# Kernel tuning notes

Measured on AMD Instinct MI355X. Metric: run time of the kernel, lower is better.

## Reference

```python
import jax, jax.numpy as jnp
import numpy as np

BLOCK_K = 128  # per_1x128 block quantization: block_n=1 (per row), block_k=128


def _dequant(wq, scale):
    # wq: [E, N, K] quantized codes; scale: [E, N, ceil(K/BLOCK_K)]
    K = wq.shape[-1]
    s_full = jnp.repeat(scale, BLOCK_K, axis=-1)[..., :K]
    return wq * s_full


def setup_inputs() -> dict:
    key = jax.random.key(0)
    ks = jax.random.split(key, 6)
    T, E, H, I = 1024, 8, 1024, 768
    x = jax.random.normal(ks[0], (T, H), dtype=jnp.float32)
    router_logits = jax.random.normal(ks[1], (T, E), dtype=jnp.float32)
    # fp8 codes simulated as float values; block scales positive (scale_inv)
    w13_weight = jax.random.normal(ks[2], (E, 2 * I, H), dtype=jnp.float32) * 0.05
    w13_weight_scale_inv = jax.random.uniform(ks[3], (E, 2 * I, H // BLOCK_K), dtype=jnp.float32, minval=0.5, maxval=1.5)
    w2_weight = jax.random.normal(ks[4], (E, H, I), dtype=jnp.float32) * 0.05
    w2_weight_scale_inv = jax.random.uniform(ks[5], (E, H, I // BLOCK_K), dtype=jnp.float32, minval=0.5, maxval=1.5)
    return {
        "x": x,
        "router_logits": router_logits,
        "w13_weight": w13_weight,
        "w13_weight_scale_inv": w13_weight_scale_inv,
        "w2_weight": w2_weight,
        "w2_weight_scale_inv": w2_weight_scale_inv,
        "top_k": 2,
    }


def reference(x, router_logits, w13_weight, w13_weight_scale_inv, w2_weight, w2_weight_scale_inv, top_k):
    T, H = x.shape
    E = router_logits.shape[-1]
    I = w2_weight.shape[-1]

    # ---- dequantize block-scaled weights (inline dequant of fp8 grouped GEMM) ----
    w13 = _dequant(w13_weight, w13_weight_scale_inv)   # [E, 2I, H]
    w2 = _dequant(w2_weight, w2_weight_scale_inv)      # [E, H, I]

    # ---- routing: softmax scoring, top_k, renormalize ----
    probs = jax.nn.softmax(router_logits, axis=-1)     # [T, E]
    topk_w, topk_idx = jax.lax.top_k(probs, top_k)     # [T, K]
    topk_w = topk_w / jnp.sum(topk_w, axis=-1, keepdims=True)  # renormalize=True
    # dense combine weights [T, E] (scatter of top_k routing weights)
    combine = jnp.zeros((T, E), x.dtype).at[jnp.arange(T)[:, None], topk_idx].add(topk_w)

    # ---- grouped expert FFN (dense-over-experts reference) ----
    gate_up = jnp.einsum('th,enh->ten', x, w13)        # [T, E, 2I]
    gate, up = gate_up[..., :I], gate_up[..., I:]
    act = jax.nn.silu(gate) * up                       # silu activation ('silu')
    out_e = jnp.einsum('tei,ehi->teh', act, w2)        # [T, E, H]

    # ---- combine ----
    return jnp.einsum('teh,te->th', out_e, combine)    # [T, H]
```

## Files before the change

### kernel.cpp

```cpp
#include <hip/hip_runtime.h>

#define T_TOK 1024
#define H_DIM 1024
#define I_DIM 768
#define E_NUM 8

#define G13 1572864
#define G2   786432
#define GX   131072
#define GO   131072

typedef __bf16 bf16x8 __attribute__((ext_vector_type(8)));
typedef float  f32x4  __attribute__((ext_vector_type(4)));

__device__ inline void gl2lds16(const void* g, void* l) {
    __builtin_amdgcn_global_load_lds(
        (const __attribute__((address_space(1))) unsigned int*)g,
        (__attribute__((address_space(3))) unsigned int*)l, 16, 0, 0);
}

__device__ inline bf16x8 cvt8(float4 a, float4 b, float s) {
    bf16x8 o;
    o[0] = (__bf16)(a.x * s); o[1] = (__bf16)(a.y * s);
    o[2] = (__bf16)(a.z * s); o[3] = (__bf16)(a.w * s);
    o[4] = (__bf16)(b.x * s); o[5] = (__bf16)(b.y * s);
    o[6] = (__bf16)(b.z * s); o[7] = (__bf16)(b.w * s);
    return o;
}

__global__ __launch_bounds__(256) void prep_kernel(
    const float* __restrict__ w13, const float* __restrict__ w13s,
    const float* __restrict__ w2,  const float* __restrict__ w2s,
    const float* __restrict__ x,   float4* __restrict__ out4,
    __bf16* __restrict__ w13d, __bf16* __restrict__ w2d, __bf16* __restrict__ xbf)
{
    int g = blockIdx.x * 256 + threadIdx.x;
    if (g < G13) {
        int k8 = g & 127;
        int row = g >> 7;
        float s = w13s[(row << 3) | (k8 >> 4)];
        const float4* src = (const float4*)w13 + (size_t)g * 2;
        *(bf16x8*)(w13d + (size_t)g * 8) = cvt8(src[0], src[1], s);
    } else if (g < G13 + G2) {
        int g2 = g - G13;
        unsigned row = (unsigned)g2 / 96u;
        int k8 = g2 - row * 96;
        float s = w2s[row * 6 + (k8 >> 4)];
        const float4* src = (const float4*)w2 + (size_t)g2 * 2;
        *(bf16x8*)(w2d + (size_t)g2 * 8) = cvt8(src[0], src[1], s);
    } else if (g < G13 + G2 + GX) {
        int gx = g - (G13 + G2);
        const float4* src = (const float4*)x + (size_t)gx * 2;
        *(bf16x8*)(xbf + (size_t)gx * 8) = cvt8(src[0], src[1], 1.0f);
    } else {
        int go = g - (G13 + G2 + GX);
        float4 z = make_float4(0.f, 0.f, 0.f, 0.f);
        out4[2 * go] = z; out4[2 * go + 1] = z;
    }
}

__global__ __launch_bounds__(1024) void router_kernel(
    const float* __restrict__ logits,
    int* __restrict__ counts, int* __restrict__ base,
    int* __restrict__ tok_list, float* __restrict__ wt_list)
{
    __shared__ int cnt[E_NUM];
    const int t = threadIdx.x;
    if (t < E_NUM) cnt[t] = 0;
    __syncthreads();
    float l[E_NUM];
#pragma unroll
    for (int e = 0; e < E_NUM; e++) l[e] = logits[t * E_NUM + e];
    int e0 = 0; float m0 = l[0];
#pragma unroll
    for (int e = 1; e < E_NUM; e++) if (l[e] > m0) { m0 = l[e]; e0 = e; }
    int e1 = -1; float m1 = -3e38f;
#pragma unroll
    for (int e = 0; e < E_NUM; e++) if (e != e0 && l[e] > m1) { m1 = l[e]; e1 = e; }
    float w0 = 1.0f / (1.0f + expf(m1 - m0));
    float w1 = 1.0f - w0;
    int p0 = atomicAdd(&cnt[e0], 1);
    tok_list[e0 * T_TOK + p0] = t;
    wt_list[e0 * T_TOK + p0] = w0;
    int p1 = atomicAdd(&cnt[e1], 1);
    tok_list[e1 * T_TOK + p1] = t;
    wt_list[e1 * T_TOK + p1] = w1;
    __syncthreads();
    if (t == 0) {
        int s = 0;
        for (int e = 0; e < E_NUM; e++) { base[e] = s; counts[e] = cnt[e]; s += cnt[e]; }
    }
}

__global__ __launch_bounds__(256, 3) void gemm1_kernel(
    const __bf16* __restrict__ xbf,
    const __bf16* __restrict__ w13d,
    const int* __restrict__ counts,
    const int* __restrict__ base,
    const int* __restrict__ tok_list,
    __bf16* __restrict__ act)
{
    const int e = blockIdx.z;
    const int count = counts[e];
    const int m0 = blockIdx.y * 32;
    if (m0 >= count) return;
    const int n0 = blockIdx.x * 64;
    const int abase = base[e];

    __shared__ union {
        struct {
            __bf16 Bs[2][128 * 64];
            __bf16 Ab[2][32 * 64];
        } s;
        float gu[32 * 132];
    } u;
    __shared__ int tokS[32];

    const int tid = threadIdx.x;
    if (tid < 32) {
        int r = m0 + tid;
        tokS[tid] = (r < count) ? tok_list[e * T_TOK + r] : tok_list[e * T_TOK];
    }
    __syncthreads();

    const int wid = tid >> 6, lane = tid & 63, lrow = lane & 15, quad = lane >> 4;

    const int rA = wid * 8 + (lane >> 3);
    const __bf16* pAst = xbf + (size_t)tokS[rA] * H_DIM + (((lane & 7) ^ (rA & 7)) << 3);
    const __bf16* pBst[4];
#pragma unroll
    for (int i8 = 0; i8 < 4; i8++) {
        int r = wid * 32 + i8 * 8 + (lane >> 3);
        int n = (r < 64) ? (n0 + r) : (I_DIM + n0 + r - 64);
        pBst[i8] = w13d + ((size_t)e * 2 * I_DIM + n) * H_DIM + (((lane & 7) ^ (r & 7)) << 3);
    }

    int aoff[2][2], boff[2][2];
#pragma unroll
    for (int kk = 0; kk < 2; kk++) {
        int gph = ((kk * 4 + quad) ^ (lrow & 7)) << 4;
#pragma unroll
        for (int i = 0; i < 2; i++) {
            aoff[kk][i] = (i * 16 + lrow) * 128 + gph;
            boff[kk][i] = (wid * 32 + i * 16 + lrow) * 128 + gph;
        }
    }

    f32x4 acc[2][2];
#pragma unroll
    for (int i = 0; i < 2; i++)
#pragma unroll
        for (int j = 0; j < 2; j++) { f32x4 z = {0.f, 0.f, 0.f, 0.f}; acc[i][j] = z; }

    auto issue = [&](int b, int k0) {
        gl2lds16(pAst + k0, &u.s.Ab[b][(wid * 8) * 64]);
#pragma unroll
        for (int i8 = 0; i8 < 4; i8++)
            gl2lds16(pBst[i8] + k0, &u.s.Bs[b][(wid * 32 + i8 * 8) * 64]);
    };
    issue(0, 0);

#pragma unroll
    for (int it = 0; it < 16; ++it) {
        const int b = it & 1;
        __syncthreads();
        if (it < 15) issue(b ^ 1, (it + 1) * 64);
        const char* Ab = (const char*)u.s.Ab[b];
        const char* Bb = (const char*)u.s.Bs[b];
#pragma unroll
        for (int kk = 0; kk < 2; kk++) {
            bf16x8 a0 = *(const bf16x8*)(Ab + aoff[kk][0]);
            bf16x8 a1 = *(const bf16x8*)(Ab + aoff[kk][1]);
            bf16x8 b0 = *(const bf16x8*)(Bb + boff[kk][0]);
            bf16x8 b1 = *(const bf16x8*)(Bb + boff[kk][1]);
            acc[0][0] = __builtin_amdgcn_mfma_f32_16x16x32_bf16(a0, b0, acc[0][0], 0, 0, 0);
            acc[1][0] = __builtin_amdgcn_mfma_f32_16x16x32_bf16(a1, b0, acc[1][0], 0, 0, 0);
            acc[0][1] = __builtin_amdgcn_mfma_f32_16x16x32_bf16(a0, b1, acc[0][1], 0, 0, 0);
            acc[1][1] = __builtin_amdgcn_mfma_f32_16x16x32_bf16(a1, b1, acc[1][1], 0, 0, 0);
        }
    }

    __syncthreads();
#pragma unroll
    for (int i = 0; i < 2; i++)
#pragma unroll
        for (int j = 0; j < 2; j++)
#pragma unroll
            for (int r = 0; r < 4; r++) {
                int m = i * 16 + quad * 4 + r;
                int c = wid * 32 + j * 16 + lrow;
                u.gu[m * 132 + c] = acc[i][j][r];
            }
    __syncthreads();

#pragma unroll
    for (int ii = 0; ii < 8; ii++) {
        int o = ii * 256 + tid;
        int m = o >> 6, c = o & 63;
        if (m0 + m < count) {
            float g  = u.gu[m * 132 + c];
            float up = u.gu[m * 132 + 64 + c];
            float a  = g / (1.0f + expf(-g)) * up;
            act[(size_t)(abase + m0 + m) * I_DIM + n0 + c] = (__bf16)a;
        }
    }
}

__global__ __launch_bounds__(256, 3) void gemm2_kernel(
    const __bf16* __restrict__ act,
    const __bf16* __restrict__ w2d,
    const int* __restrict__ counts,
    const int* __restrict__ base,
    const int* __restrict__ tok_list,
    const float* __restrict__ wt_list,
    float* __restrict__ out)
{
    const int e = blockIdx.z;
    const int count = counts[e];
    const int m0 = blockIdx.y * 32;
    if (m0 >= count) return;
    const int n0 = blockIdx.x * 128;
    const int abase = base[e];

    __shared__ struct {
        __bf16 Bs[2][128 * 64];
        __bf16 Ab[2][32 * 64];
    } s;
    __shared__ int   tokS[32];
    __shared__ float wtS[32];

    const int tid = threadIdx.x;
    if (tid < 32) {
        int r = m0 + tid;
        tokS[tid] = (r < count) ? tok_list[e * T_TOK + r] : tok_list[e * T_TOK];
        wtS[tid]  = (r < count) ? wt_list[e * T_TOK + r] : 0.f;
    }
    __syncthreads();

    const int wid = tid >> 6, lane = tid & 63, lrow = lane & 15, quad = lane >> 4;

    const int rA = wid * 8 + (lane >> 3);
    int gr = abase + m0 + rA;
    if (gr > 2 * T_TOK - 1) gr = 2 * T_TOK - 1;
    const __bf16* pAst = act + (size_t)gr * I_DIM + (((lane & 7) ^ (rA & 7)) << 3);
    const __bf16* pBst[4];
#pragma unroll
    for (int i8 = 0; i8 < 4; i8++) {
        int r = wid * 32 + i8 * 8 + (lane >> 3);
        pBst[i8] = w2d + ((size_t)e * H_DIM + n0 + r) * I_DIM + (((lane & 7) ^ (r & 7)) << 3);
    }

    int aoff[2][2], boff[2][2];
#pragma unroll
    for (int kk = 0; kk < 2; kk++) {
        int gph = ((kk * 4 + quad) ^ (lrow & 7)) << 4;
#pragma unroll
        for (int i = 0; i < 2; i++) {
            aoff[kk][i] = (i * 16 + lrow) * 128 + gph;
            boff[kk][i] = (wid * 32 + i * 16 + lrow) * 128 + gph;
        }
    }

    f32x4 acc[2][2];
#pragma unroll
    for (int i = 0; i < 2; i++)
#pragma unroll
        for (int j = 0; j < 2; j++) { f32x4 z = {0.f, 0.f, 0.f, 0.f}; acc[i][j] = z; }

    auto issue = [&](int b, int k0) {
        gl2lds16(pAst + k0, &s.Ab[b][(wid * 8) * 64]);
#pragma unroll
        for (int i8 = 0; i8 < 4; i8++)
            gl2lds16(pBst[i8] + k0, &s.Bs[b][(wid * 32 + i8 * 8) * 64]);
    };
    issue(0, 0);

#pragma unroll
    for (int it = 0; it < 12; ++it) {
        const int b = it & 1;
        __syncthreads();
        if (it < 11) issue(b ^ 1, (it + 1) * 64);
        const char* Ab = (const char*)s.Ab[b];
        const char* Bb = (const char*)s.Bs[b];
#pragma unroll
        for (int kk = 0; kk < 2; kk++) {
            bf16x8 a0 = *(const bf16x8*)(Ab + aoff[kk][0]);
            bf16x8 a1 = *(const bf16x8*)(Ab + aoff[kk][1]);
            bf16x8 b0 = *(const bf16x8*)(Bb + boff[kk][0]);
            bf16x8 b1 = *(const bf16x8*)(Bb + boff[kk][1]);
            acc[0][0] = __builtin_amdgcn_mfma_f32_16x16x32_bf16(a0, b0, acc[0][0], 0, 0, 0);
            acc[1][0] = __builtin_amdgcn_mfma_f32_16x16x32_bf16(a1, b0, acc[1][0], 0, 0, 0);
            acc[0][1] = __builtin_amdgcn_mfma_f32_16x16x32_bf16(a0, b1, acc[0][1], 0, 0, 0);
            acc[1][1] = __builtin_amdgcn_mfma_f32_16x16x32_bf16(a1, b1, acc[1][1], 0, 0, 0);
        }
    }

#pragma unroll
    for (int i = 0; i < 2; i++)
#pragma unroll
        for (int j = 0; j < 2; j++)
#pragma unroll
            for (int r = 0; r < 4; r++) {
                int m = i * 16 + quad * 4 + r;
                if (m0 + m < count) {
                    int h = n0 + wid * 32 + j * 16 + lrow;
                    atomicAdd(&out[(size_t)tokS[m] * H_DIM + h], wtS[m] * acc[i][j][r]);
                }
            }
}

extern "C" void kernel_launch(void* const* d_in, const int* in_sizes, int n_in,
                              void* d_out, int out_size, void* d_ws, size_t ws_size,
                              hipStream_t stream) {
    (void)in_sizes; (void)n_in; (void)out_size; (void)ws_size;
    const float* x      = (const float*)d_in[0];
    const float* logits = (const float*)d_in[1];
    const float* w13    = (const float*)d_in[2];
    const float* w13s   = (const float*)d_in[3];
    const float* w2     = (const float*)d_in[4];
    const float* w2s    = (const float*)d_in[5];
    float* out = (float*)d_out;

    char* ws = (char*)d_ws;
    int*    counts   = (int*)ws;
    int*    base     = (int*)(ws + 128);
    int*    tok_list = (int*)(ws + 256);
    float*  wt_list  = (float*)(ws + 256 + 32768);
    __bf16* act      = (__bf16*)(ws + 65792);
    __bf16* xbf      = (__bf16*)(ws + 65792 + 3145728);
    __bf16* w13d     = (__bf16*)(ws + 65792 + 3145728 + 2097152);
    __bf16* w2d      = (__bf16*)(ws + 65792 + 3145728 + 2097152 + 25165824);

    prep_kernel<<<dim3(10240), 256, 0, stream>>>(w13, w13s, w2, w2s, x,
                                                 (float4*)out, w13d, w2d, xbf);
    router_kernel<<<dim3(1), 1024, 0, stream>>>(logits, counts, base, tok_list, wt_list);
    gemm1_kernel<<<dim3(I_DIM / 64, T_TOK / 32, E_NUM), 256, 0, stream>>>(
        xbf, w13d, counts, base, tok_list, act);
    gemm2_kernel<<<dim3(H_DIM / 128, T_TOK / 32, E_NUM), 256, 0, stream>>>(
        act, w2d, counts, base, tok_list, wt_list, out);
}
```

Before: 162.6 us.

## Replace direct global-to-LDS loads with register-staged double-buffered prefetch in GEMMs

Both grouped GEMM kernels stop using the direct global-to-LDS load builtin. They now prefetch tiles two stages ahead into registers and write them to swizzled LDS with an extra barrier per iteration. Occupancy hints rise from 3 to 4 blocks per CU. In gemm2, token IDs and weights are read straight from global memory in the epilogue instead of staged in shared memory. The intent is deeper latency hiding and higher occupancy, at the cost of more registers, an additional sync per k-step and VGPR-to-LDS store traffic.

```diff
diff --git a/kernel.cpp b/kernel.cpp
--- a/kernel.cpp
+++ b/kernel.cpp
@@ -8,16 +8,9 @@
 #define G13 1572864
 #define G2   786432
 #define GX   131072
-#define GO   131072
 
 typedef __bf16 bf16x8 __attribute__((ext_vector_type(8)));
 typedef float  f32x4  __attribute__((ext_vector_type(4)));
-
-__device__ inline void gl2lds16(const void* g, void* l) {
-    __builtin_amdgcn_global_load_lds(
-        (const __attribute__((address_space(1))) unsigned int*)g,
-        (__attribute__((address_space(3))) unsigned int*)l, 16, 0, 0);
-}
 
 __device__ inline bf16x8 cvt8(float4 a, float4 b, float s) {
     bf16x8 o;
@@ -92,7 +85,9 @@
     }
 }
 
-__global__ __launch_bounds__(256, 3) void gemm1_kernel(
+#define MFMA(A, B, C) __builtin_amdgcn_mfma_f32_16x16x32_bf16(A, B, C, 0, 0, 0)
+
+__global__ __launch_bounds__(256, 4) void gemm1_kernel(
     const __bf16* __restrict__ xbf,
     const __bf16* __restrict__ w13d,
     const int* __restrict__ counts,
@@ -108,33 +103,30 @@
     const int abase = base[e];
 
     __shared__ union {
-        struct {
-            __bf16 Bs[2][128 * 64];
-            __bf16 Ab[2][32 * 64];
-        } s;
+        struct { __bf16 Bs[2][128 * 64]; __bf16 As[2][32 * 64]; } s;
         float gu[32 * 132];
+        int tok[32];
     } u;
-    __shared__ int tokS[32];
 
     const int tid = threadIdx.x;
     if (tid < 32) {
         int r = m0 + tid;
-        tokS[tid] = (r < count) ? tok_list[e * T_TOK + r] : tok_list[e * T_TOK];
-    }
-    __syncthreads();
+        u.tok[tid] = (r < count) ? tok_list[e * T_TOK + r] : tok_list[e * T_TOK];
+    }
+    __syncthreads();
+
+    const int arow = tid >> 3, ag = tid & 7;
+    const __bf16* pA = xbf + (size_t)u.tok[arow] * H_DIM + ag * 8;
+    const int awo = arow * 128 + ((ag ^ (arow & 7)) << 4);
+    const int brow = tid >> 1, bg0 = (tid & 1) * 4;
+    const int nB = (brow < 64) ? (n0 + brow) : (I_DIM + n0 + brow - 64);
+    const __bf16* pB = w13d + ((size_t)e * 2 * I_DIM + nB) * H_DIM + bg0 * 8;
+    int bwo[4];
+#pragma unroll
+    for (int i = 0; i < 4; i++)
+        bwo[i] = brow * 128 + (((bg0 + i) ^ (brow & 7)) << 4);
 
     const int wid = tid >> 6, lane = tid & 63, lrow = lane & 15, quad = lane >> 4;
-
-    const int rA = wid * 8 + (lane >> 3);
-    const __bf16* pAst = xbf + (size_t)tokS[rA] * H_DIM + (((lane & 7) ^ (rA & 7)) << 3);
-    const __bf16* pBst[4];
-#pragma unroll
-    for (int i8 = 0; i8 < 4; i8++) {
-        int r = wid * 32 + i8 * 8 + (lane >> 3);
-        int n = (r < 64) ? (n0 + r) : (I_DIM + n0 + r - 64);
-        pBst[i8] = w13d + ((size_t)e * 2 * I_DIM + n) * H_DIM + (((lane & 7) ^ (r & 7)) << 3);
-    }
-
     int aoff[2][2], boff[2][2];
 #pragma unroll
     for (int kk = 0; kk < 2; kk++) {
@@ -152,20 +144,32 @@
 #pragma unroll
         for (int j = 0; j < 2; j++) { f32x4 z = {0.f, 0.f, 0.f, 0.f}; acc[i][j] = z; }
 
-    auto issue = [&](int b, int k0) {
-        gl2lds16(pAst + k0, &u.s.Ab[b][(wid * 8) * 64]);
-#pragma unroll
-        for (int i8 = 0; i8 < 4; i8++)
-            gl2lds16(pBst[i8] + k0, &u.s.Bs[b][(wid * 32 + i8 * 8) * 64]);
-    };
-    issue(0, 0);
-
-#pragma unroll
+    uint4 rA[2], rB[2][4];
+#pragma unroll
+    for (int s = 0; s < 2; s++) {
+        rA[s] = *(const uint4*)(pA + s * 64);
+#pragma unroll
+        for (int i = 0; i < 4; i++)
+            rB[s][i] = *(const uint4*)(pB + s * 64 + i * 8);
+    }
+
+#pragma unroll 2
     for (int it = 0; it < 16; ++it) {
         const int b = it & 1;
         __syncthreads();
-        if (it < 15) issue(b ^ 1, (it + 1) * 64);
-        const char* Ab = (const char*)u.s.Ab[b];
+        *(uint4*)((char*)u.s.As[b] + awo) = rA[b];
+#pragma unroll
+        for (int i = 0; i < 4; i++)
+            *(uint4*)((char*)u.s.Bs[b] + bwo[i]) = rB[b][i];
+        if (it + 2 < 16) {
+            const int k = (it + 2) * 64;
+            rA[b] = *(const uint4*)(pA + k);
+#pragma unroll
+            for (int i = 0; i < 4; i++)
+                rB[b][i] = *(const uint4*)(pB + k + i * 8);
+        }
+        __syncthreads();
+        const char* Ab = (const char*)u.s.As[b];
         const char* Bb = (const char*)u.s.Bs[b];
 #pragma unroll
         for (int kk = 0; kk < 2; kk++) {
@@ -173,10 +177,10 @@
             bf16x8 a1 = *(const bf16x8*)(Ab + aoff[kk][1]);
             bf16x8 b0 = *(const bf16x8*)(Bb + boff[kk][0]);
             bf16x8 b1 = *(const bf16x8*)(Bb + boff[kk][1]);
-            acc[0][0] = __builtin_amdgcn_mfma_f32_16x16x32_bf16(a0, b0, acc[0][0], 0, 0, 0);
-            acc[1][0] = __builtin_amdgcn_mfma_f32_16x16x32_bf16(a1, b0, acc[1][0], 0, 0, 0);
-            acc[0][1] = __builtin_amdgcn_mfma_f32_16x16x32_bf16(a0, b1, acc[0][1], 0, 0, 0);
-            acc[1][1] = __builtin_amdgcn_mfma_f32_16x16x32_bf16(a1, b1, acc[1][1], 0, 0, 0);
+            acc[0][0] = MFMA(a0, b0, acc[0][0]);
+            acc[1][0] = MFMA(a1, b0, acc[1][0]);
+            acc[0][1] = MFMA(a0, b1, acc[0][1]);
+            acc[1][1] = MFMA(a1, b1, acc[1][1]);
         }
     }
 
@@ -206,7 +210,7 @@
     }
 }
 
-__global__ __launch_bounds__(256, 3) void gemm2_kernel(
+__global__ __launch_bounds__(256, 4) void gemm2_kernel(
     const __bf16* __restrict__ act,
     const __bf16* __restrict__ w2d,
     const int* __restrict__ counts,
@@ -222,34 +226,24 @@
     const int n0 = blockIdx.x * 128;
     const int abase = base[e];
 
-    __shared__ struct {
-        __bf16 Bs[2][128 * 64];
-        __bf16 Ab[2][32 * 64];
-    } s;
-    __shared__ int   tokS[32];
-    __shared__ float wtS[32];
+    __shared__ struct { __bf16 Bs[2][128 * 64]; __bf16 As[2][32 * 64]; } s;
 
     const int tid = threadIdx.x;
-    if (tid < 32) {
-        int r = m0 + tid;
-        tokS[tid] = (r < count) ? tok_list[e * T_TOK + r] : tok_list[e * T_TOK];
-        wtS[tid]  = (r < count) ? wt_list[e * T_TOK + r] : 0.f;
-    }
-    __syncthreads();
+
+    const int arow = tid >> 3, ag = tid & 7;
+    int gr = abase + m0 + arow;
+    if (gr > 2 * T_TOK - 1) gr = 2 * T_TOK - 1;
+    const __bf16* pA = act + (size_t)gr * I_DIM + ag * 8;
+    const int awo = arow * 128 + ((ag ^ (arow & 7)) << 4);
+
+    const int brow = tid >> 1, bg0 = (tid & 1) * 4;
+    const __bf16* pB = w2d + ((size_t)e * H_DIM + n0 + brow) * I_DIM + bg0 * 8;
+    int bwo[4];
+#pragma unroll
+    for (int i = 0; i < 4; i++)
+        bwo[i] = brow * 128 + (((bg0 + i) ^ (brow & 7)) << 4);
 
     const int wid = tid >> 6, lane = tid & 63, lrow = lane & 15, quad = lane >> 4;
-
-    const int rA = wid * 8 + (lane >> 3);
-    int gr = abase + m0 + rA;
-    if (gr > 2 * T_TOK - 1) gr = 2 * T_TOK - 1;
-    const __bf16* pAst = act + (size_t)gr * I_DIM + (((lane & 7) ^ (rA & 7)) << 3);
-    const __bf16* pBst[4];
-#pragma unroll
-    for (int i8 = 0; i8 < 4; i8++) {
-        int r = wid * 32 + i8 * 8 + (lane >> 3);
-        pBst[i8] = w2d + ((size_t)e * H_DIM + n0 + r) * I_DIM + (((lane & 7) ^ (r & 7)) << 3);
-    }
-
     int aoff[2][2], boff[2][2];
 #pragma unroll
     for (int kk = 0; kk < 2; kk++) {
@@ -267,20 +261,32 @@
 #pragma unroll
         for (int j = 0; j < 2; j++) { f32x4 z = {0.f, 0.f, 0.f, 0.f}; acc[i][j] = z; }
 
-    auto issue = [&](int b, int k0) {
-        gl2lds16(pAst + k0, &s.Ab[b][(wid * 8) * 64]);
-#pragma unroll
-        for (int i8 = 0; i8 < 4; i8++)
-            gl2lds16(pBst[i8] + k0, &s.Bs[b][(wid * 32 + i8 * 8) * 64]);
-    };
-    issue(0, 0);
-
-#pragma unroll
+    uint4 rA[2], rB[2][4];
+#pragma unroll
+    for (int sdeep = 0; sdeep < 2; sdeep++) {
+        rA[sdeep] = *(const uint4*)(pA + sdeep * 64);
+#pragma unroll
+        for (int i = 0; i < 4; i++)
+            rB[sdeep][i] = *(const uint4*)(pB + sdeep * 64 + i * 8);
+    }
+
+#pragma unroll 2
     for (int it = 0; it < 12; ++it) {
         const int b = it & 1;
         __syncthreads();
-        if (it < 11) issue(b ^ 1, (it + 1) * 64);
-        const char* Ab = (const char*)s.Ab[b];
+        *(uint4*)((char*)s.As[b] + awo) = rA[b];
+#pragma unroll
+        for (int i = 0; i < 4; i++)
+            *(uint4*)((char*)s.Bs[b] + bwo[i]) = rB[b][i];
+        if (it + 2 < 12) {
+            const int k = (it + 2) * 64;
+            rA[b] = *(const uint4*)(pA + k);
+#pragma unroll
+            for (int i = 0; i < 4; i++)
+                rB[b][i] = *(const uint4*)(pB + k + i * 8);
+        }
+        __syncthreads();
+        const char* Ab = (const char*)s.As[b];
         const char* Bb = (const char*)s.Bs[b];
 #pragma unroll
         for (int kk = 0; kk < 2; kk++) {
@@ -288,25 +294,28 @@
             bf16x8 a1 = *(const bf16x8*)(Ab + aoff[kk][1]);
             bf16x8 b0 = *(const bf16x8*)(Bb + boff[kk][0]);
             bf16x8 b1 = *(const bf16x8*)(Bb + boff[kk][1]);
-            acc[0][0] = __builtin_amdgcn_mfma_f32_16x16x32_bf16(a0, b0, acc[0][0], 0, 0, 0);
-            acc[1][0] = __builtin_amdgcn_mfma_f32_16x16x32_bf16(a1, b0, acc[1][0], 0, 0, 0);
-            acc[0][1] = __builtin_amdgcn_mfma_f32_16x16x32_bf16(a0, b1, acc[0][1], 0, 0, 0);
-            acc[1][1] = __builtin_amdgcn_mfma_f32_16x16x32_bf16(a1, b1, acc[1][1], 0, 0, 0);
+            acc[0][0] = MFMA(a0, b0, acc[0][0]);
+            acc[1][0] = MFMA(a1, b0, acc[1][0]);
+            acc[0][1] = MFMA(a0, b1, acc[0][1]);
+            acc[1][1] = MFMA(a1, b1, acc[1][1]);
         }
     }
 
 #pragma unroll
     for (int i = 0; i < 2; i++)
 #pragma unroll
-        for (int j = 0; j < 2; j++)
-#pragma unroll
-            for (int r = 0; r < 4; r++) {
-                int m = i * 16 + quad * 4 + r;
-                if (m0 + m < count) {
+        for (int r = 0; r < 4; r++) {
+            int m = i * 16 + quad * 4 + r;
+            if (m0 + m < count) {
+                int   t = tok_list[e * T_TOK + m0 + m];
+                float w = wt_list[e * T_TOK + m0 + m];
+#pragma unroll
+                for (int j = 0; j < 2; j++) {
                     int h = n0 + wid * 32 + j * 16 + lrow;
-                    atomicAdd(&out[(size_t)tokS[m] * H_DIM + h], wtS[m] * acc[i][j][r]);
+                    atomicAdd(&out[(size_t)t * H_DIM + h], w * acc[i][j][r]);
                 }
             }
+        }
 }
 
 extern "C" void kernel_launch(void* const* d_in, const int* in_sizes, int n_in,
```

New measurement: 294.2 us. 1.81x slower.
